# Kernel optimization log

Measured on AMD Instinct MI355X. Metric: run time of the kernel, lower is better.

The kernel has to match this reference:

```python
import jax, jax.numpy as jnp
import numpy as np

BS, N, J, F = 8, 1024, 4, 32
N_CLASSES = 2


def setup_inputs() -> dict:
    key = jax.random.key(0)
    k1, k2, k3, k4 = jax.random.split(key, 4)
    WW = jax.random.normal(k1, (BS, N, N, J), dtype=jnp.float32)
    x = jax.random.normal(k2, (BS, N, F), dtype=jnp.float32)
    # nn.Linear(J*F, n_classes): weight (n_classes, J*F), bias (n_classes,)
    bound = 1.0 / np.sqrt(J * F)
    fc_w = jax.random.uniform(k3, (N_CLASSES, J * F), minval=-bound, maxval=bound, dtype=jnp.float32)
    fc_b = jax.random.uniform(k4, (N_CLASSES,), minval=-bound, maxval=bound, dtype=jnp.float32)
    return {"WW": WW, "x": x, "fc_w": fc_w, "fc_b": fc_b}


def reference(WW, x, fc_w, fc_b):
    bs, n, _, j = WW.shape
    f = x.shape[-1]
    # GMul: out[b,n,j*F+f] = sum_m W[b,n,m,j] * x[b,m,f]
    h = jnp.einsum('bnmj,bmf->bnjf', WW, x).reshape(bs, n, j * f)
    # Linear over last dim
    out = h @ fc_w.T + fc_b  # (bs, N, n_classes)
    return out
```

## Files before the change

kernel.cpp:

```cpp
#include <hip/hip_runtime.h>

#define BS 8
#define NN 1024
#define JJ 4
#define FF 32
#define NC 2

typedef float f4v __attribute__((ext_vector_type(4)));

__global__ void __launch_bounds__(1024) fused_gmul_fc_kernel(
    const float* __restrict__ WW, const float* __restrict__ x,
    const float* __restrict__ fc_w, const float* __restrict__ fc_b,
    float* __restrict__ out) {
    __shared__ float4 lyA[NN];
    __shared__ float4 lyB[NN];

    const int blk  = blockIdx.x;
    const int b    = blk >> 5;
    const int tid  = threadIdx.x;
    const int wave = tid >> 6;
    const int lane = tid & 63;

    {
        const float4* xr =
            reinterpret_cast<const float4*>(x + ((size_t)b * NN + tid) * FF);
        float xv[FF];
#pragma unroll
        for (int q = 0; q < FF / 4; ++q) {
            float4 v = xr[q];
            xv[q * 4 + 0] = v.x; xv[q * 4 + 1] = v.y;
            xv[q * 4 + 2] = v.z; xv[q * 4 + 3] = v.w;
        }
        float a00 = 0.f, a01 = 0.f, a10 = 0.f, a11 = 0.f;
        float a20 = 0.f, a21 = 0.f, a30 = 0.f, a31 = 0.f;
        const float* w0 = fc_w;
        const float* w1 = fc_w + JJ * FF;
#pragma unroll
        for (int f = 0; f < FF; ++f) {
            float xf = xv[f];
            a00 += xf * w0[0 * FF + f];  a01 += xf * w1[0 * FF + f];
            a10 += xf * w0[1 * FF + f];  a11 += xf * w1[1 * FF + f];
            a20 += xf * w0[2 * FF + f];  a21 += xf * w1[2 * FF + f];
            a30 += xf * w0[3 * FF + f];  a31 += xf * w1[3 * FF + f];
        }
        lyA[tid] = make_float4(a00, a01, a10, a11);
        lyB[tid] = make_float4(a20, a21, a30, a31);
    }
    __syncthreads();

    const int row0 = blk * 32 + wave * 2;
    const f4v* W0 = reinterpret_cast<const f4v*>(WW) + (size_t)row0 * NN;
    const f4v* W1 = W0 + NN;

    float s00 = 0.f, s01 = 0.f, s10 = 0.f, s11 = 0.f;
#pragma unroll 4
    for (int m = lane; m < NN; m += 64) {
        f4v w0 = W0[m];
        f4v w1 = W1[m];
        float4 ya = lyA[m];
        float4 yb = lyB[m];
        s00 += w0.x * ya.x + w0.y * ya.z + w0.z * yb.x + w0.w * yb.z;
        s01 += w0.x * ya.y + w0.y * ya.w + w0.z * yb.y + w0.w * yb.w;
        s10 += w1.x * ya.x + w1.y * ya.z + w1.z * yb.x + w1.w * yb.z;
        s11 += w1.x * ya.y + w1.y * ya.w + w1.z * yb.y + w1.w * yb.w;
    }
#pragma unroll
    for (int off = 32; off > 0; off >>= 1) {
        s00 += __shfl_down(s00, off, 64);
        s01 += __shfl_down(s01, off, 64);
        s10 += __shfl_down(s10, off, 64);
        s11 += __shfl_down(s11, off, 64);
    }
    if (lane == 0) {
        float b0 = fc_b[0], b1 = fc_b[1];
        out[(size_t)row0 * NC + 0] = s00 + b0;
        out[(size_t)row0 * NC + 1] = s01 + b1;
        out[(size_t)(row0 + 1) * NC + 0] = s10 + b0;
        out[(size_t)(row0 + 1) * NC + 1] = s11 + b1;
    }
}

extern "C" void kernel_launch(void* const* d_in, const int* in_sizes, int n_in,
                              void* d_out, int out_size, void* d_ws, size_t ws_size,
                              hipStream_t stream) {
    const float* WW   = (const float*)d_in[0];
    const float* x    = (const float*)d_in[1];
    const float* fc_w = (const float*)d_in[2];
    const float* fc_b = (const float*)d_in[3];
    float* out = (float*)d_out;

    int blocks = (BS * NN) / 32;
    fused_gmul_fc_kernel<<<blocks, 1024, 0, stream>>>(WW, x, fc_w, fc_b, out);
}
```

Before: 33.34 us.

## Split reduction over m into chunks with atomic accumulation and nontemporal loads

Restructures the kernel so each 256-thread block handles 16 rows over one quarter of the m dimension, instead of 32 rows over all of m with 1024 threads. Each block computes the x·fc_w projection only for its 256-row chunk of x, which cuts the redundant projection work per block. Partial sums go to the output through atomicAdd after a memset, and WW is read with nontemporal loads. In exchange it adds a memset launch, atomic traffic, and results that depend on summation order.

```diff
diff --git a/kernel.cpp b/kernel.cpp
--- a/kernel.cpp
+++ b/kernel.cpp
@@ -6,77 +6,93 @@
 #define FF 32
 #define NC 2
 
+#define CHUNK 256
+#define NCHUNK (NN / CHUNK)
+#define ROWS 16
+#define THREADS 256
+
 typedef float f4v __attribute__((ext_vector_type(4)));
 
-__global__ void __launch_bounds__(1024) fused_gmul_fc_kernel(
+__global__ void __launch_bounds__(THREADS) fused_atomic_kernel(
     const float* __restrict__ WW, const float* __restrict__ x,
     const float* __restrict__ fc_w, const float* __restrict__ fc_b,
     float* __restrict__ out) {
-    __shared__ float4 lyA[NN];
-    __shared__ float4 lyB[NN];
+    __shared__ float4 lyA[CHUNK];
+    __shared__ float4 lyB[CHUNK];
 
-    const int blk  = blockIdx.x;
-    const int b    = blk >> 5;
+    const int bid    = blockIdx.x;
+    const int chunk  = bid & (NCHUNK - 1);
+    const int rowgrp = bid >> 2;
+    const int b      = rowgrp >> 6;
+    const int m0     = chunk * CHUNK;
+
     const int tid  = threadIdx.x;
     const int wave = tid >> 6;
     const int lane = tid & 63;
 
     {
-        const float4* xr =
-            reinterpret_cast<const float4*>(x + ((size_t)b * NN + tid) * FF);
+        const float4* xr = reinterpret_cast<const float4*>(
+            x + ((size_t)b * NN + m0 + tid) * FF);
         float xv[FF];
 #pragma unroll
         for (int q = 0; q < FF / 4; ++q) {
             float4 v = xr[q];
-            xv[q * 4 + 0] = v.x; xv[q * 4 + 1] = v.y;
-            xv[q * 4 + 2] = v.z; xv[q * 4 + 3] = v.w;
+            xv[4 * q + 0] = v.x; xv[4 * q + 1] = v.y;
+            xv[4 * q + 2] = v.z; xv[4 * q + 3] = v.w;
         }
-        float a00 = 0.f, a01 = 0.f, a10 = 0.f, a11 = 0.f;
-        float a20 = 0.f, a21 = 0.f, a30 = 0.f, a31 = 0.f;
-        const float* w0 = fc_w;
-        const float* w1 = fc_w + JJ * FF;
+        float a[JJ][NC];
 #pragma unroll
-        for (int f = 0; f < FF; ++f) {
-            float xf = xv[f];
-            a00 += xf * w0[0 * FF + f];  a01 += xf * w1[0 * FF + f];
-            a10 += xf * w0[1 * FF + f];  a11 += xf * w1[1 * FF + f];
-            a20 += xf * w0[2 * FF + f];  a21 += xf * w1[2 * FF + f];
-            a30 += xf * w0[3 * FF + f];  a31 += xf * w1[3 * FF + f];
+        for (int j = 0; j < JJ; ++j) {
+            float s0 = 0.f, s1 = 0.f;
+            const float* w0 = fc_w + 0 * (JJ * FF) + j * FF;
+            const float* w1 = fc_w + 1 * (JJ * FF) + j * FF;
+#pragma unroll
+            for (int f = 0; f < FF; ++f) {
+                float xf = xv[f];
+                s0 += xf * w0[f];
+                s1 += xf * w1[f];
+            }
+            a[j][0] = s0; a[j][1] = s1;
         }
-        lyA[tid] = make_float4(a00, a01, a10, a11);
-        lyB[tid] = make_float4(a20, a21, a30, a31);
+        lyA[tid] = make_float4(a[0][0], a[0][1], a[1][0], a[1][1]);
+        lyB[tid] = make_float4(a[2][0], a[2][1], a[3][0], a[3][1]);
     }
     __syncthreads();
 
-    const int row0 = blk * 32 + wave * 2;
-    const f4v* W0 = reinterpret_cast<const f4v*>(WW) + (size_t)row0 * NN;
-    const f4v* W1 = W0 + NN;
+    const int row0 = rowgrp * ROWS + wave * 4;
+    const f4v* Wp = reinterpret_cast<const f4v*>(WW);
 
-    float s00 = 0.f, s01 = 0.f, s10 = 0.f, s11 = 0.f;
-#pragma unroll 4
-    for (int m = lane; m < NN; m += 64) {
-        f4v w0 = W0[m];
-        f4v w1 = W1[m];
-        float4 ya = lyA[m];
-        float4 yb = lyB[m];
-        s00 += w0.x * ya.x + w0.y * ya.z + w0.z * yb.x + w0.w * yb.z;
-        s01 += w0.x * ya.y + w0.y * ya.w + w0.z * yb.y + w0.w * yb.w;
-        s10 += w1.x * ya.x + w1.y * ya.z + w1.z * yb.x + w1.w * yb.z;
-        s11 += w1.x * ya.y + w1.y * ya.w + w1.z * yb.y + w1.w * yb.w;
+    float s[4][2] = {{0.f, 0.f}, {0.f, 0.f}, {0.f, 0.f}, {0.f, 0.f}};
+#pragma unroll
+    for (int i = 0; i < CHUNK / 64; ++i) {
+        const int ml = lane + 64 * i;
+        const float4 ya = lyA[ml];
+        const float4 yb = lyB[ml];
+        const size_t base = (size_t)row0 * NN + m0 + ml;
+#pragma unroll
+        for (int r = 0; r < 4; ++r) {
+            f4v w = __builtin_nontemporal_load(Wp + base + (size_t)r * NN);
+            s[r][0] += w.x * ya.x + w.y * ya.z + w.z * yb.x + w.w * yb.z;
+            s[r][1] += w.x * ya.y + w.y * ya.w + w.z * yb.y + w.w * yb.w;
+        }
     }
+
 #pragma unroll
     for (int off = 32; off > 0; off >>= 1) {
-        s00 += __shfl_down(s00, off, 64);
-        s01 += __shfl_down(s01, off, 64);
-        s10 += __shfl_down(s10, off, 64);
-        s11 += __shfl_down(s11, off, 64);
+#pragma unroll
+        for (int r = 0; r < 4; ++r) {
+            s[r][0] += __shfl_down(s[r][0], off, 64);
+            s[r][1] += __shfl_down(s[r][1], off, 64);
+        }
     }
     if (lane == 0) {
-        float b0 = fc_b[0], b1 = fc_b[1];
-        out[(size_t)row0 * NC + 0] = s00 + b0;
-        out[(size_t)row0 * NC + 1] = s01 + b1;
-        out[(size_t)(row0 + 1) * NC + 0] = s10 + b0;
-        out[(size_t)(row0 + 1) * NC + 1] = s11 + b1;
+        const float b0 = (chunk == 0) ? fc_b[0] : 0.f;
+        const float b1 = (chunk == 0) ? fc_b[1] : 0.f;
+#pragma unroll
+        for (int r = 0; r < 4; ++r) {
+            atomicAdd(&out[(size_t)(row0 + r) * NC + 0], s[r][0] + b0);
+            atomicAdd(&out[(size_t)(row0 + r) * NC + 1], s[r][1] + b1);
+        }
     }
 }
 
@@ -89,6 +105,8 @@
     const float* fc_b = (const float*)d_in[3];
     float* out = (float*)d_out;
 
-    int blocks = (BS * NN) / 32;
-    fused_gmul_fc_kernel<<<blocks, 1024, 0, stream>>>(WW, x, fc_w, fc_b, out);
+    hipMemsetAsync(out, 0, (size_t)out_size * sizeof(float), stream);
+
+    const int blocks = (BS * NN / ROWS) * NCHUNK;
+    fused_atomic_kernel<<<blocks, THREADS, 0, stream>>>(WW, x, fc_w, fc_b, out);
 }
```

Result: slower. 39.24 us (+17.7%).
